# Kernel tuning notes

Measured on AMD Instinct MI355X. Metric: run time of the kernel, lower is better.

Reference implementation:

```python
import jax, jax.numpy as jnp
import numpy as np

STEP_NUM = 2
SAMPLE_NUM = 10
SAMPLE_SCOPE = 128
NODE_NUM = 232965
INPUT_DIM = 602
HIDDEN_DIM = 256
OUTPUT_DIM = 41
BATCH = 256


def _forward(ids, feature, edge, weight, sample_W, sample_W2, sample_a, W1, W2):
    # a: softmax over the 3 mixing coefficients (matches softmax_a(sample_a) then mm)
    a = jax.nn.softmax(sample_a, axis=0)[:, 0]  # [3]
    key = jax.random.key(42)
    adj_list = [None] * STEP_NUM
    in_nodes = ids
    for i in range(STEP_NUM):
        layer = STEP_NUM - 1 - i
        nbr = edge[in_nodes]              # [n, S] candidate neighbor ids
        src_f = feature[in_nodes]         # [n, F]
        tgt_f = feature[nbr]              # [n, S, F]
        # GAT-style bilinear attention scores (two heads) + structural weight
        s1 = src_f @ sample_W             # [n, H]
        s2 = src_f @ sample_W2            # [n, H]
        t1 = jnp.einsum('nsf,fh->nsh', tgt_f, sample_W)   # [n, S, H]
        t2 = jnp.einsum('nsf,fh->nsh', tgt_f, sample_W2)  # [n, S, H]
        att1 = jnp.einsum('nh,nsh->ns', s1, t1)
        att2 = jnp.einsum('nh,nsh->ns', s2, t2)
        att3 = weight[in_nodes]           # [n, S]
        att = jax.nn.relu(a[0] * att1 + a[1] * att2 + a[2] * att3) + 1e-9
        # Categorical sampling of SAMPLE_NUM neighbors per node
        key, sk = jax.random.split(key)
        cols = jax.random.categorical(sk, jnp.log(att), shape=(SAMPLE_NUM, in_nodes.shape[0])).T  # [n, K]
        # sub-graph adjacency: row-normalized sampled weights (block-sparse structure)
        w = jnp.take_along_axis(weight[in_nodes], cols, axis=1)  # [n, K]
        adj_list[layer] = w / (w.sum(axis=1, keepdims=True) + 1e-9)
        in_nodes = jnp.take_along_axis(nbr, cols, axis=1).reshape(-1)  # [n*K]
    X = feature[in_nodes]                 # start_feat: deepest frontier features
    Ws = [W1, W2]
    for layer in range(STEP_NUM):
        n = adj_list[layer].shape[0]
        # sparse adjacency matmul == per-row weighted sum over sampled neighbors
        X = jnp.einsum('nk,nkd->nd', adj_list[layer], X.reshape(n, SAMPLE_NUM, -1))
        X = X @ Ws[layer]
        if layer < STEP_NUM - 1:
            X = jax.nn.relu(X)  # dropout is identity in eval
    return X


def setup_inputs() -> dict:
    key = jax.random.key(0)
    ks = jax.random.split(key, 9)
    N1 = NODE_NUM + 1
    return {
        'ids': jax.random.randint(ks[0], (BATCH,), 0, NODE_NUM),
        'feature': jax.random.normal(ks[1], (N1, INPUT_DIM), dtype=jnp.float32),
        'edge': jax.random.randint(ks[2], (N1, SAMPLE_SCOPE), 0, NODE_NUM),
        'weight': jax.random.uniform(ks[3], (N1, SAMPLE_SCOPE), dtype=jnp.float32),
        'sample_W': jax.random.normal(ks[4], (INPUT_DIM, HIDDEN_DIM), dtype=jnp.float32) * 0.05,
        'sample_W2': jax.random.normal(ks[5], (INPUT_DIM, HIDDEN_DIM), dtype=jnp.float32) * 0.05,
        'sample_a': jax.random.normal(ks[6], (3, 1), dtype=jnp.float32),
        'W1': jax.random.normal(ks[7], (INPUT_DIM, HIDDEN_DIM), dtype=jnp.float32) * 0.05,
        'W2': jax.random.normal(ks[8], (HIDDEN_DIM, OUTPUT_DIM), dtype=jnp.float32) * 0.05,
    }


def reference(ids, feature, edge, weight, sample_W, sample_W2, sample_a, W1, W2):
    return _forward(ids, feature, edge, weight, sample_W, sample_W2, sample_a, W1, W2)
```

## Files before the change

### kernel.cpp

```cpp
#include <hip/hip_runtime.h>
#include <cstdint>
#include <cstddef>

#define JAX_PARTITIONABLE 1

#define S_SCOPE 128
#define K_SAMP  10
#define F_DIM   602
#define H_DIM   256
#define O_DIM   41
#define BATCH_N 256

__host__ __device__ __forceinline__ void tf2x32(uint32_t k0, uint32_t k1,
                                                uint32_t x0, uint32_t x1,
                                                uint32_t* o0, uint32_t* o1) {
  uint32_t ks2 = k0 ^ k1 ^ 0x1BD11BDAu;
  x0 += k0; x1 += k1;
#define TF_R(d) { x0 += x1; x1 = (x1 << (d)) | (x1 >> (32 - (d))); x1 ^= x0; }
#define TF_G0 TF_R(13) TF_R(15) TF_R(26) TF_R(6)
#define TF_G1 TF_R(17) TF_R(29) TF_R(16) TF_R(24)
  TF_G0; x0 += k1;  x1 += ks2 + 1u;
  TF_G1; x0 += ks2; x1 += k0  + 2u;
  TF_G0; x0 += k0;  x1 += k1  + 3u;
  TF_G1; x0 += k1;  x1 += ks2 + 4u;
  TF_G0; x0 += ks2; x1 += k0  + 5u;
#undef TF_R
#undef TF_G0
#undef TF_G1
  *o0 = x0; *o1 = x1;
}

__device__ __forceinline__ float jax_gumbel(uint32_t ka, uint32_t kb, uint32_t j, uint32_t M) {
  uint32_t r0, r1, bits;
#if JAX_PARTITIONABLE
  tf2x32(ka, kb, 0u, j, &r0, &r1);
  bits = r0 ^ r1;
#else
  uint32_t half = M >> 1;
  if (j < half) { tf2x32(ka, kb, j, j + half, &r0, &r1); bits = r0; }
  else          { tf2x32(ka, kb, j - half, j, &r0, &r1); bits = r1; }
#endif
  float f = __uint_as_float((bits >> 9) | 0x3f800000u) - 1.0f;
  if (f == 0.0f) f = 1.17549435e-38f;
  return -logf(-logf(f));
}

template<int R>
__global__ void __launch_bounds__(256) k_sg(const float* __restrict__ feature,
                                            const float* __restrict__ Wa,
                                            const float* __restrict__ Wb,
                                            const int* __restrict__ nodes,
                                            float* __restrict__ g1,
                                            float* __restrict__ g2) {
  __shared__ __align__(16) float fl[R][604];
  __shared__ __align__(16) float sl[R][H_DIM];
  const float* __restrict__ W = blockIdx.y ? Wb : Wa;
  float* __restrict__ g = blockIdx.y ? g2 : g1;
  const int r0 = blockIdx.x * R;
  const int tid = threadIdx.x;
  for (int r = 0; r < R; ++r) {
    const float* src = feature + (size_t)nodes[r0 + r] * F_DIM;
    for (int e = tid; e < 604; e += 256) fl[r][e] = (e < F_DIM) ? src[e] : 0.f;
  }
  __syncthreads();

  {
    const int h = tid;
    float a[R];
#pragma unroll
    for (int r = 0; r < R; ++r) a[r] = 0.f;
    for (int fc = 0; fc < 150; ++fc) {
      const int f = fc * 4;
      const float w0 = W[(size_t)(f + 0) * H_DIM + h];
      const float w1 = W[(size_t)(f + 1) * H_DIM + h];
      const float w2 = W[(size_t)(f + 2) * H_DIM + h];
      const float w3 = W[(size_t)(f + 3) * H_DIM + h];
#pragma unroll
      for (int r = 0; r < R; ++r) {
        const float4 v = *(const float4*)&fl[r][f];
        a[r] = fmaf(v.x, w0, a[r]); a[r] = fmaf(v.y, w1, a[r]);
        a[r] = fmaf(v.z, w2, a[r]); a[r] = fmaf(v.w, w3, a[r]);
      }
    }
    for (int f = 600; f < 602; ++f) {
      const float w = W[(size_t)f * H_DIM + h];
#pragma unroll
      for (int r = 0; r < R; ++r) a[r] = fmaf(fl[r][f], w, a[r]);
    }
#pragma unroll
    for (int r = 0; r < R; ++r) sl[r][h] = a[r];
  }
  __syncthreads();

  for (int j = 0; j < 3; ++j) {
    const int f = tid + j * 256;
    if (f < F_DIM) {
      const float4* wr = (const float4*)(W + (size_t)f * H_DIM);
      float b[R];
#pragma unroll
      for (int r = 0; r < R; ++r) b[r] = 0.f;
      for (int hq = 0; hq < H_DIM / 4; ++hq) {
        const float4 w = wr[hq];
#pragma unroll
        for (int r = 0; r < R; ++r) {
          const float4 v = *(const float4*)&sl[r][hq * 4];
          b[r] = fmaf(v.x, w.x, b[r]); b[r] = fmaf(v.y, w.y, b[r]);
          b[r] = fmaf(v.z, w.z, b[r]); b[r] = fmaf(v.w, w.w, b[r]);
        }
      }
#pragma unroll
      for (int r = 0; r < R; ++r)
        g[(size_t)(r0 + r) * F_DIM + f] = b[r];
    }
  }
}

template<int FUSE_Y, int BLK>
__global__ void __launch_bounds__(BLK) k_att(const float* __restrict__ feature,
                                             const int* __restrict__ edge,
                                             const float* __restrict__ weight,
                                             const float* __restrict__ g1,
                                             const float* __restrict__ g2,
                                             const int* __restrict__ nodes,
                                             int n,
                                             const float* __restrict__ sample_a,
                                             uint32_t ska, uint32_t skb,
                                             float* __restrict__ adj_or_y,
                                             int* __restrict__ out_nodes) {
  constexpr int NW = BLK / 64;
  __shared__ __align__(16) float g1l[602];
  __shared__ __align__(16) float g2l[602];
  __shared__ float logitl[S_SCOPE];
  __shared__ float wtl[S_SCOPE];
  __shared__ int nbrl[S_SCOPE];
  __shared__ int coll[K_SAMP];
  __shared__ float selw[K_SAMP];
  __shared__ int selr[K_SAMP];

  const int nIdx = blockIdx.x;
  const int tid = threadIdx.x;
  const int lane = tid & 63;
  const int wave = tid >> 6;
  const int node = nodes[nIdx];

  const float a0v = sample_a[0], a1v = sample_a[1], a2v = sample_a[2];
  const float mx = fmaxf(a0v, fmaxf(a1v, a2v));
  const float e0 = expf(a0v - mx), e1 = expf(a1v - mx), e2 = expf(a2v - mx);
  const float inv = 1.0f / (e0 + e1 + e2);
  const float aw0 = e0 * inv, aw1 = e1 * inv, aw2 = e2 * inv;

  for (int e = tid; e < F_DIM; e += BLK) {
    g1l[e] = g1[(size_t)nIdx * F_DIM + e];
    g2l[e] = g2[(size_t)nIdx * F_DIM + e];
  }
  __syncthreads();

  for (int t16 = 0; t16 < S_SCOPE / (2 * NW); ++t16) {
    const int sA = wave + t16 * (2 * NW);
    const int sB = sA + NW;
    const int nbrA = edge[(size_t)node * S_SCOPE + sA];
    const int nbrB = edge[(size_t)node * S_SCOPE + sB];
    const float wtA = weight[(size_t)node * S_SCOPE + sA];
    const float wtB = weight[(size_t)node * S_SCOPE + sB];
    const float2* frA = (const float2*)(feature + (size_t)nbrA * F_DIM);
    const float2* frB = (const float2*)(feature + (size_t)nbrB * F_DIM);
    float2 vA[5], vB[5], gav[5], gbv[5];
#pragma unroll
    for (int t = 0; t < 5; ++t) {
      const int p = lane + t * 64;
      if (p < F_DIM / 2) {
        vA[t] = frA[p]; vB[t] = frB[p];
        gav[t] = ((const float2*)g1l)[p];
        gbv[t] = ((const float2*)g2l)[p];
      } else {
        vA[t] = make_float2(0.f, 0.f); vB[t] = make_float2(0.f, 0.f);
        gav[t] = make_float2(0.f, 0.f); gbv[t] = make_float2(0.f, 0.f);
      }
    }
    float d1A = 0.f, d2A = 0.f, d1B = 0.f, d2B = 0.f;
#pragma unroll
    for (int t = 0; t < 5; ++t) {
      d1A = fmaf(vA[t].x, gav[t].x, fmaf(vA[t].y, gav[t].y, d1A));
      d2A = fmaf(vA[t].x, gbv[t].x, fmaf(vA[t].y, gbv[t].y, d2A));
      d1B = fmaf(vB[t].x, gav[t].x, fmaf(vB[t].y, gav[t].y, d1B));
      d2B = fmaf(vB[t].x, gbv[t].x, fmaf(vB[t].y, gbv[t].y, d2B));
    }
#pragma unroll
    for (int off = 32; off > 0; off >>= 1) {
      d1A += __shfl_xor(d1A, off); d2A += __shfl_xor(d2A, off);
      d1B += __shfl_xor(d1B, off); d2B += __shfl_xor(d2B, off);
    }
    if (lane == 0) {
      const float attA = fmaxf(aw0 * d1A + aw1 * d2A + aw2 * wtA, 0.0f) + 1e-9f;
      const float attB = fmaxf(aw0 * d1B + aw1 * d2B + aw2 * wtB, 0.0f) + 1e-9f;
      logitl[sA] = logf(attA); wtl[sA] = wtA; nbrl[sA] = nbrA;
      logitl[sB] = logf(attB); wtl[sB] = wtB; nbrl[sB] = nbrB;
    }
  }
  __syncthreads();

  const uint32_t M = (uint32_t)K_SAMP * (uint32_t)n * (uint32_t)S_SCOPE;
  for (int k = wave; k < K_SAMP; k += NW) {
    const uint32_t jbase = ((uint32_t)k * (uint32_t)n + (uint32_t)nIdx) * (uint32_t)S_SCOPE;
    float v0 = logitl[lane]      + jax_gumbel(ska, skb, jbase + (uint32_t)lane,        M);
    float v1 = logitl[lane + 64] + jax_gumbel(ska, skb, jbase + (uint32_t)(lane + 64), M);
    float best = v0; int bidx = lane;
    if (v1 > best) { best = v1; bidx = lane + 64; }
#pragma unroll
    for (int off = 1; off < 64; off <<= 1) {
      const float ov = __shfl_xor(best, off);
      const int oi = __shfl_xor(bidx, off);
      if (ov > best || (ov == best && oi < bidx)) { best = ov; bidx = oi; }
    }
    if (lane == 0) coll[k] = bidx;
  }
  __syncthreads();

  if constexpr (FUSE_Y) {
    if (tid == 0) {
      float w[K_SAMP]; float sum = 0.f;
#pragma unroll
      for (int k = 0; k < K_SAMP; ++k) { w[k] = wtl[coll[k]]; sum += w[k]; }
      const float den = sum + 1e-9f;
#pragma unroll
      for (int k = 0; k < K_SAMP; ++k) {
        selw[k] = w[k] / den;
        selr[k] = nbrl[coll[k]];
      }
    }
    __syncthreads();
    for (int e = tid; e < F_DIM; e += BLK) {
      float acc = 0.f;
#pragma unroll
      for (int k = 0; k < K_SAMP; ++k)
        acc = fmaf(selw[k], feature[(size_t)selr[k] * F_DIM + e], acc);
      adj_or_y[(size_t)nIdx * F_DIM + e] = acc;
    }
  } else {
    if (tid == 0) {
      float w[K_SAMP]; float sum = 0.f;
#pragma unroll
      for (int k = 0; k < K_SAMP; ++k) { w[k] = wtl[coll[k]]; sum += w[k]; }
      const float den = sum + 1e-9f;
#pragma unroll
      for (int k = 0; k < K_SAMP; ++k) {
        adj_or_y[(size_t)nIdx * K_SAMP + k] = w[k] / den;
        out_nodes[nIdx * K_SAMP + k] = nbrl[coll[k]];
      }
    }
  }
}

#define HROWS 4
__global__ void __launch_bounds__(256) k_h(const float* __restrict__ y,
                                           const float* __restrict__ W1,
                                           float* __restrict__ H) {
  __shared__ __align__(16) float yl[HROWS][604];
  const int r0 = blockIdx.x * HROWS;
  const int tid = threadIdx.x;
  for (int r = 0; r < HROWS; ++r)
    for (int e = tid; e < 604; e += 256)
      yl[r][e] = (e < F_DIM) ? y[(size_t)(r0 + r) * F_DIM + e] : 0.f;
  __syncthreads();
  const int h = tid;
  float acc[HROWS];
#pragma unroll
  for (int r = 0; r < HROWS; ++r) acc[r] = 0.f;
  for (int fc = 0; fc < 150; ++fc) {
    const int f = fc * 4;
    const float w0 = W1[(size_t)(f + 0) * H_DIM + h];
    const float w1 = W1[(size_t)(f + 1) * H_DIM + h];
    const float w2 = W1[(size_t)(f + 2) * H_DIM + h];
    const float w3 = W1[(size_t)(f + 3) * H_DIM + h];
#pragma unroll
    for (int r = 0; r < HROWS; ++r) {
      const float4 v = *(const float4*)&yl[r][f];
      acc[r] = fmaf(v.x, w0, acc[r]); acc[r] = fmaf(v.y, w1, acc[r]);
      acc[r] = fmaf(v.z, w2, acc[r]); acc[r] = fmaf(v.w, w3, acc[r]);
    }
  }
  for (int f = 600; f < 602; ++f) {
    const float w = W1[(size_t)f * H_DIM + h];
#pragma unroll
    for (int r = 0; r < HROWS; ++r) acc[r] = fmaf(yl[r][f], w, acc[r]);
  }
#pragma unroll
  for (int r = 0; r < HROWS; ++r)
    H[(size_t)(r0 + r) * H_DIM + h] = fmaxf(acc[r], 0.f);
}

__global__ void __launch_bounds__(256) k_final(const float* __restrict__ H,
                                               const float* __restrict__ adj1,
                                               const float* __restrict__ W2,
                                               float* __restrict__ out) {
  __shared__ float zl[H_DIM];
  const int nIdx = blockIdx.x;
  const int tid = threadIdx.x;
  float acc = 0.f;
#pragma unroll
  for (int k = 0; k < K_SAMP; ++k)
    acc = fmaf(adj1[(size_t)nIdx * K_SAMP + k],
               H[(size_t)(nIdx * K_SAMP + k) * H_DIM + tid], acc);
  zl[tid] = acc;
  __syncthreads();
  if (tid < O_DIM) {
    float o = 0.f;
    for (int hh = 0; hh < H_DIM; ++hh)
      o = fmaf(zl[hh], W2[(size_t)hh * O_DIM + tid], o);
    out[(size_t)nIdx * O_DIM + tid] = o;
  }
}

extern "C" void kernel_launch(void* const* d_in, const int* in_sizes, int n_in,
                              void* d_out, int out_size, void* d_ws, size_t ws_size,
                              hipStream_t stream) {
  (void)in_sizes; (void)n_in; (void)out_size; (void)ws_size;
  const int*   ids       = (const int*)d_in[0];
  const float* feature   = (const float*)d_in[1];
  const int*   edge      = (const int*)d_in[2];
  const float* weight    = (const float*)d_in[3];
  const float* sample_W  = (const float*)d_in[4];
  const float* sample_W2 = (const float*)d_in[5];
  const float* sample_a  = (const float*)d_in[6];
  const float* W1        = (const float*)d_in[7];
  const float* W2        = (const float*)d_in[8];
  float* out = (float*)d_out;

  const int N1 = BATCH_N;
  const int N2 = BATCH_N * K_SAMP;

  float* ws   = (float*)d_ws;
  float* g1   = ws;
  float* g2   = g1 + (size_t)N2 * F_DIM;
  float* yb   = g2 + (size_t)N2 * F_DIM;
  float* Hb   = yb + (size_t)N2 * F_DIM;
  float* adj1 = Hb + (size_t)N2 * H_DIM;
  int*   in1  = (int*)(adj1 + (size_t)N1 * K_SAMP);

  uint32_t k0 = 0u, k1 = 42u;
  uint32_t nk0, nk1, sk0a, sk0b, sk1a, sk1b;
#if JAX_PARTITIONABLE
  {
    tf2x32(k0, k1, 0u, 0u, &nk0, &nk1);
    tf2x32(k0, k1, 0u, 1u, &sk0a, &sk0b);
    tf2x32(nk0, nk1, 0u, 1u, &sk1a, &sk1b);
  }
#else
  {
    uint32_t a0, b0, a1, b1;
    tf2x32(k0, k1, 0u, 2u, &a0, &b0);
    tf2x32(k0, k1, 1u, 3u, &a1, &b1);
    nk0 = a0; nk1 = a1; sk0a = b0; sk0b = b1;
    tf2x32(nk0, nk1, 0u, 2u, &a0, &b0);
    tf2x32(nk0, nk1, 1u, 3u, &a1, &b1);
    sk1a = b0; sk1b = b1;
  }
#endif

  k_sg<2><<<dim3(N1 / 2, 2), 256, 0, stream>>>(feature, sample_W, sample_W2, ids, g1, g2);
  k_att<0, 1024><<<N1, 1024, 0, stream>>>(feature, edge, weight, g1, g2, ids, N1,
                                          sample_a, sk0a, sk0b, adj1, in1);
  k_sg<10><<<dim3(N2 / 10, 2), 256, 0, stream>>>(feature, sample_W, sample_W2, in1, g1, g2);
  k_att<1, 512><<<N2, 512, 0, stream>>>(feature, edge, weight, g1, g2, in1, N2,
                                        sample_a, sk1a, sk1b, yb, nullptr);
  k_h<<<N2 / HROWS, 256, 0, stream>>>(yb, W1, Hb);
  k_final<<<N1, 256, 0, stream>>>(Hb, adj1, W2, out);
}
```

Baseline: 369.9 us.

## Fuse layer-0 projection with attention, pipeline neighbor loads, fuse output kernels

Merges the first-hop sg projection into the first attention kernel, so each block computes its own g1/g2 vectors in shared memory. The attention core now preloads edge and weight rows once and double-buffers the neighbor feature rows, overlapping the next row's load with the current dot product. It also fuses the hidden projection, ReLU, weighted aggregation and output matmul into one kernel, removing the H buffer round trip. The cost is redundant W reads per block in the fused layer-0 kernel and the 1024-thread layer-0 launch being cut to 512 threads.

```diff
diff --git a/kernel.cpp b/kernel.cpp
--- a/kernel.cpp
+++ b/kernel.cpp
@@ -45,6 +45,224 @@
   return -logf(-logf(f));
 }
 
+__device__ __forceinline__ void cand_load(const float* __restrict__ feature,
+                                          int nbr, int lane, float2* buf) {
+  const float2* fr = (const float2*)(feature + (size_t)nbr * F_DIM);
+#pragma unroll
+  for (int t = 0; t < 5; ++t) {
+    const int p = lane + t * 64;
+    buf[t] = (p < F_DIM / 2) ? fr[p] : make_float2(0.f, 0.f);
+  }
+}
+
+__device__ __forceinline__ void cand_dot(const float2* buf,
+                                         const float* g1l, const float* g2l,
+                                         int lane, float& d1, float& d2) {
+  d1 = 0.f; d2 = 0.f;
+#pragma unroll
+  for (int t = 0; t < 5; ++t) {
+    const int p = lane + t * 64;
+    float2 ga, gb;
+    if (p < F_DIM / 2) {
+      ga = ((const float2*)g1l)[p];
+      gb = ((const float2*)g2l)[p];
+    } else {
+      ga = make_float2(0.f, 0.f);
+      gb = make_float2(0.f, 0.f);
+    }
+    d1 = fmaf(buf[t].x, ga.x, fmaf(buf[t].y, ga.y, d1));
+    d2 = fmaf(buf[t].x, gb.x, fmaf(buf[t].y, gb.y, d2));
+  }
+}
+
+__device__ __forceinline__ void red2(float& d1, float& d2) {
+#pragma unroll
+  for (int off = 32; off > 0; off >>= 1) {
+    d1 += __shfl_xor(d1, off);
+    d2 += __shfl_xor(d2, off);
+  }
+}
+
+template<int FUSE_Y>
+__device__ __forceinline__ void att_core(const float* __restrict__ feature,
+                                         const float* g1l, const float* g2l,
+                                         float* logitl, float* wtl, int* nbrl,
+                                         int* coll, float* selw, int* selr,
+                                         int nIdx, int n,
+                                         float aw0, float aw1, float aw2,
+                                         uint32_t ska, uint32_t skb,
+                                         float* __restrict__ adj_or_y,
+                                         int* __restrict__ out_nodes) {
+  constexpr int BLK = 512;
+  constexpr int NW = BLK / 64;
+  constexpr int NIT = S_SCOPE / NW;
+  const int tid = threadIdx.x;
+  const int lane = tid & 63;
+  const int wave = tid >> 6;
+
+  float2 bufA[5], bufB[5];
+  cand_load(feature, nbrl[wave], lane, bufA);
+  for (int it = 0; it < NIT; it += 2) {
+    const int sA = wave + it * NW;
+    const int sB = sA + NW;
+    cand_load(feature, nbrl[sB], lane, bufB);
+    {
+      float d1, d2;
+      cand_dot(bufA, g1l, g2l, lane, d1, d2);
+      red2(d1, d2);
+      if (lane == 0) {
+        const float att = fmaxf(aw0 * d1 + aw1 * d2 + aw2 * wtl[sA], 0.0f) + 1e-9f;
+        logitl[sA] = logf(att);
+      }
+    }
+    if (it + 2 < NIT) cand_load(feature, nbrl[sB + NW], lane, bufA);
+    {
+      float d1, d2;
+      cand_dot(bufB, g1l, g2l, lane, d1, d2);
+      red2(d1, d2);
+      if (lane == 0) {
+        const float att = fmaxf(aw0 * d1 + aw1 * d2 + aw2 * wtl[sB], 0.0f) + 1e-9f;
+        logitl[sB] = logf(att);
+      }
+    }
+  }
+  __syncthreads();
+
+  const uint32_t M = (uint32_t)K_SAMP * (uint32_t)n * (uint32_t)S_SCOPE;
+  for (int k = wave; k < K_SAMP; k += NW) {
+    const uint32_t jbase = ((uint32_t)k * (uint32_t)n + (uint32_t)nIdx) * (uint32_t)S_SCOPE;
+    float v0 = logitl[lane]      + jax_gumbel(ska, skb, jbase + (uint32_t)lane,        M);
+    float v1 = logitl[lane + 64] + jax_gumbel(ska, skb, jbase + (uint32_t)(lane + 64), M);
+    float best = v0; int bidx = lane;
+    if (v1 > best) { best = v1; bidx = lane + 64; }
+#pragma unroll
+    for (int off = 1; off < 64; off <<= 1) {
+      const float ov = __shfl_xor(best, off);
+      const int oi = __shfl_xor(bidx, off);
+      if (ov > best || (ov == best && oi < bidx)) { best = ov; bidx = oi; }
+    }
+    if (lane == 0) coll[k] = bidx;
+  }
+  __syncthreads();
+
+  if constexpr (FUSE_Y) {
+    if (tid == 0) {
+      float w[K_SAMP]; float sum = 0.f;
+#pragma unroll
+      for (int k = 0; k < K_SAMP; ++k) { w[k] = wtl[coll[k]]; sum += w[k]; }
+      const float den = sum + 1e-9f;
+#pragma unroll
+      for (int k = 0; k < K_SAMP; ++k) {
+        selw[k] = w[k] / den;
+        selr[k] = nbrl[coll[k]];
+      }
+    }
+    __syncthreads();
+    for (int e = tid; e < F_DIM; e += BLK) {
+      float acc = 0.f;
+#pragma unroll
+      for (int k = 0; k < K_SAMP; ++k)
+        acc = fmaf(selw[k], feature[(size_t)selr[k] * F_DIM + e], acc);
+      adj_or_y[(size_t)nIdx * F_DIM + e] = acc;
+    }
+  } else {
+    if (tid == 0) {
+      float w[K_SAMP]; float sum = 0.f;
+#pragma unroll
+      for (int k = 0; k < K_SAMP; ++k) { w[k] = wtl[coll[k]]; sum += w[k]; }
+      const float den = sum + 1e-9f;
+#pragma unroll
+      for (int k = 0; k < K_SAMP; ++k) {
+        adj_or_y[(size_t)nIdx * K_SAMP + k] = w[k] / den;
+        out_nodes[nIdx * K_SAMP + k] = nbrl[coll[k]];
+      }
+    }
+  }
+}
+
+__global__ void __launch_bounds__(512) k_sgatt0(const float* __restrict__ feature,
+                                                const int* __restrict__ edge,
+                                                const float* __restrict__ weight,
+                                                const float* __restrict__ Wa,
+                                                const float* __restrict__ Wb,
+                                                const int* __restrict__ nodes,
+                                                int n,
+                                                const float* __restrict__ sample_a,
+                                                uint32_t ska, uint32_t skb,
+                                                float* __restrict__ adj,
+                                                int* __restrict__ out_nodes) {
+  __shared__ __align__(16) float fl[604];
+  __shared__ __align__(16) float sl[2][H_DIM];
+  __shared__ __align__(16) float g1l[604];
+  __shared__ __align__(16) float g2l[604];
+  __shared__ float logitl[S_SCOPE];
+  __shared__ float wtl[S_SCOPE];
+  __shared__ int nbrl[S_SCOPE];
+  __shared__ int coll[K_SAMP];
+
+  const int nIdx = blockIdx.x;
+  const int tid = threadIdx.x;
+  const int node = nodes[nIdx];
+
+  const float a0v = sample_a[0], a1v = sample_a[1], a2v = sample_a[2];
+  const float mx = fmaxf(a0v, fmaxf(a1v, a2v));
+  const float e0 = expf(a0v - mx), e1 = expf(a1v - mx), e2 = expf(a2v - mx);
+  const float inv = 1.0f / (e0 + e1 + e2);
+  const float aw0 = e0 * inv, aw1 = e1 * inv, aw2 = e2 * inv;
+
+  {
+    const float* src = feature + (size_t)node * F_DIM;
+    for (int e = tid; e < 604; e += 512) fl[e] = (e < F_DIM) ? src[e] : 0.f;
+    if (tid < S_SCOPE) {
+      nbrl[tid] = edge[(size_t)node * S_SCOPE + tid];
+      wtl[tid] = weight[(size_t)node * S_SCOPE + tid];
+    }
+  }
+  __syncthreads();
+
+  {
+    const int head = tid >> 8;
+    const int h = tid & 255;
+    const float* __restrict__ W = head ? Wb : Wa;
+    float a = 0.f;
+    for (int fc = 0; fc < 150; ++fc) {
+      const int f = fc * 4;
+      const float w0 = W[(size_t)(f + 0) * H_DIM + h];
+      const float w1 = W[(size_t)(f + 1) * H_DIM + h];
+      const float w2 = W[(size_t)(f + 2) * H_DIM + h];
+      const float w3 = W[(size_t)(f + 3) * H_DIM + h];
+      const float4 v = *(const float4*)&fl[f];
+      a = fmaf(v.x, w0, a); a = fmaf(v.y, w1, a);
+      a = fmaf(v.z, w2, a); a = fmaf(v.w, w3, a);
+    }
+    for (int f = 600; f < 602; ++f) a = fmaf(fl[f], W[(size_t)f * H_DIM + h], a);
+    sl[head][h] = a;
+  }
+  __syncthreads();
+
+  for (int j = 0; j < 3; ++j) {
+    const int idx = tid + j * 512;
+    if (idx < 2 * F_DIM) {
+      const int head = idx >= F_DIM;
+      const int f = head ? idx - F_DIM : idx;
+      const float* __restrict__ W = head ? Wb : Wa;
+      const float4* wr = (const float4*)(W + (size_t)f * H_DIM);
+      float b = 0.f;
+      for (int hq = 0; hq < H_DIM / 4; ++hq) {
+        const float4 w = wr[hq];
+        const float4 v = *(const float4*)&sl[head][hq * 4];
+        b = fmaf(v.x, w.x, b); b = fmaf(v.y, w.y, b);
+        b = fmaf(v.z, w.z, b); b = fmaf(v.w, w.w, b);
+      }
+      (head ? g2l : g1l)[f] = b;
+    }
+  }
+  __syncthreads();
+
+  att_core<0>(feature, g1l, g2l, logitl, wtl, nbrl, coll, nullptr, nullptr,
+              nIdx, n, aw0, aw1, aw2, ska, skb, adj, out_nodes);
+}
+
 template<int R>
 __global__ void __launch_bounds__(256) k_sg(const float* __restrict__ feature,
                                             const float* __restrict__ Wa,
@@ -115,21 +333,18 @@
   }
 }
 
-template<int FUSE_Y, int BLK>
-__global__ void __launch_bounds__(BLK) k_att(const float* __restrict__ feature,
-                                             const int* __restrict__ edge,
-                                             const float* __restrict__ weight,
-                                             const float* __restrict__ g1,
-                                             const float* __restrict__ g2,
-                                             const int* __restrict__ nodes,
-                                             int n,
-                                             const float* __restrict__ sample_a,
-                                             uint32_t ska, uint32_t skb,
-                                             float* __restrict__ adj_or_y,
-                                             int* __restrict__ out_nodes) {
-  constexpr int NW = BLK / 64;
-  __shared__ __align__(16) float g1l[602];
-  __shared__ __align__(16) float g2l[602];
+__global__ void __launch_bounds__(512) k_att1(const float* __restrict__ feature,
+                                              const int* __restrict__ edge,
+                                              const float* __restrict__ weight,
+                                              const float* __restrict__ g1,
+                                              const float* __restrict__ g2,
+                                              const int* __restrict__ nodes,
+                                              int n,
+                                              const float* __restrict__ sample_a,
+                                              uint32_t ska, uint32_t skb,
+                                              float* __restrict__ y) {
+  __shared__ __align__(16) float g1l[604];
+  __shared__ __align__(16) float g2l[604];
   __shared__ float logitl[S_SCOPE];
   __shared__ float wtl[S_SCOPE];
   __shared__ int nbrl[S_SCOPE];
@@ -139,8 +354,6 @@
 
   const int nIdx = blockIdx.x;
   const int tid = threadIdx.x;
-  const int lane = tid & 63;
-  const int wave = tid >> 6;
   const int node = nodes[nIdx];
 
   const float a0v = sample_a[0], a1v = sample_a[1], a2v = sample_a[2];
@@ -149,123 +362,39 @@
   const float inv = 1.0f / (e0 + e1 + e2);
   const float aw0 = e0 * inv, aw1 = e1 * inv, aw2 = e2 * inv;
 
-  for (int e = tid; e < F_DIM; e += BLK) {
+  for (int e = tid; e < F_DIM; e += 512) {
     g1l[e] = g1[(size_t)nIdx * F_DIM + e];
     g2l[e] = g2[(size_t)nIdx * F_DIM + e];
   }
-  __syncthreads();
-
-  for (int t16 = 0; t16 < S_SCOPE / (2 * NW); ++t16) {
-    const int sA = wave + t16 * (2 * NW);
-    const int sB = sA + NW;
-    const int nbrA = edge[(size_t)node * S_SCOPE + sA];
-    const int nbrB = edge[(size_t)node * S_SCOPE + sB];
-    const float wtA = weight[(size_t)node * S_SCOPE + sA];
-    const float wtB = weight[(size_t)node * S_SCOPE + sB];
-    const float2* frA = (const float2*)(feature + (size_t)nbrA * F_DIM);
-    const float2* frB = (const float2*)(feature + (size_t)nbrB * F_DIM);
-    float2 vA[5], vB[5], gav[5], gbv[5];
-#pragma unroll
-    for (int t = 0; t < 5; ++t) {
-      const int p = lane + t * 64;
-      if (p < F_DIM / 2) {
-        vA[t] = frA[p]; vB[t] = frB[p];
-        gav[t] = ((const float2*)g1l)[p];
-        gbv[t] = ((const float2*)g2l)[p];
-      } else {
-        vA[t] = make_float2(0.f, 0.f); vB[t] = make_float2(0.f, 0.f);
-        gav[t] = make_float2(0.f, 0.f); gbv[t] = make_float2(0.f, 0.f);
-      }
-    }
-    float d1A = 0.f, d2A = 0.f, d1B = 0.f, d2B = 0.f;
-#pragma unroll
-    for (int t = 0; t < 5; ++t) {
-      d1A = fmaf(vA[t].x, gav[t].x, fmaf(vA[t].y, gav[t].y, d1A));
-      d2A = fmaf(vA[t].x, gbv[t].x, fmaf(vA[t].y, gbv[t].y, d2A));
-      d1B = fmaf(vB[t].x, gav[t].x, fmaf(vB[t].y, gav[t].y, d1B));
-      d2B = fmaf(vB[t].x, gbv[t].x, fmaf(vB[t].y, gbv[t].y, d2B));
-    }
-#pragma unroll
-    for (int off = 32; off > 0; off >>= 1) {
-      d1A += __shfl_xor(d1A, off); d2A += __shfl_xor(d2A, off);
-      d1B += __shfl_xor(d1B, off); d2B += __shfl_xor(d2B, off);
-    }
-    if (lane == 0) {
-      const float attA = fmaxf(aw0 * d1A + aw1 * d2A + aw2 * wtA, 0.0f) + 1e-9f;
-      const float attB = fmaxf(aw0 * d1B + aw1 * d2B + aw2 * wtB, 0.0f) + 1e-9f;
-      logitl[sA] = logf(attA); wtl[sA] = wtA; nbrl[sA] = nbrA;
-      logitl[sB] = logf(attB); wtl[sB] = wtB; nbrl[sB] = nbrB;
-    }
-  }
-  __syncthreads();
-
-  const uint32_t M = (uint32_t)K_SAMP * (uint32_t)n * (uint32_t)S_SCOPE;
-  for (int k = wave; k < K_SAMP; k += NW) {
-    const uint32_t jbase = ((uint32_t)k * (uint32_t)n + (uint32_t)nIdx) * (uint32_t)S_SCOPE;
-    float v0 = logitl[lane]      + jax_gumbel(ska, skb, jbase + (uint32_t)lane,        M);
-    float v1 = logitl[lane + 64] + jax_gumbel(ska, skb, jbase + (uint32_t)(lane + 64), M);
-    float best = v0; int bidx = lane;
-    if (v1 > best) { best = v1; bidx = lane + 64; }
-#pragma unroll
-    for (int off = 1; off < 64; off <<= 1) {
-      const float ov = __shfl_xor(best, off);
-      const int oi = __shfl_xor(bidx, off);
-      if (ov > best || (ov == best && oi < bidx)) { best = ov; bidx = oi; }
-    }
-    if (lane == 0) coll[k] = bidx;
-  }
-  __syncthreads();
-
-  if constexpr (FUSE_Y) {
-    if (tid == 0) {
-      float w[K_SAMP]; float sum = 0.f;
-#pragma unroll
-      for (int k = 0; k < K_SAMP; ++k) { w[k] = wtl[coll[k]]; sum += w[k]; }
-      const float den = sum + 1e-9f;
-#pragma unroll
-      for (int k = 0; k < K_SAMP; ++k) {
-        selw[k] = w[k] / den;
-        selr[k] = nbrl[coll[k]];
-      }
-    }
-    __syncthreads();
-    for (int e = tid; e < F_DIM; e += BLK) {
-      float acc = 0.f;
-#pragma unroll
-      for (int k = 0; k < K_SAMP; ++k)
-        acc = fmaf(selw[k], feature[(size_t)selr[k] * F_DIM + e], acc);
-      adj_or_y[(size_t)nIdx * F_DIM + e] = acc;
-    }
-  } else {
-    if (tid == 0) {
-      float w[K_SAMP]; float sum = 0.f;
-#pragma unroll
-      for (int k = 0; k < K_SAMP; ++k) { w[k] = wtl[coll[k]]; sum += w[k]; }
-      const float den = sum + 1e-9f;
-#pragma unroll
-      for (int k = 0; k < K_SAMP; ++k) {
-        adj_or_y[(size_t)nIdx * K_SAMP + k] = w[k] / den;
-        out_nodes[nIdx * K_SAMP + k] = nbrl[coll[k]];
-      }
-    }
-  }
-}
-
-#define HROWS 4
-__global__ void __launch_bounds__(256) k_h(const float* __restrict__ y,
-                                           const float* __restrict__ W1,
-                                           float* __restrict__ H) {
-  __shared__ __align__(16) float yl[HROWS][604];
-  const int r0 = blockIdx.x * HROWS;
+  if (tid < S_SCOPE) {
+    nbrl[tid] = edge[(size_t)node * S_SCOPE + tid];
+    wtl[tid] = weight[(size_t)node * S_SCOPE + tid];
+  }
+  __syncthreads();
+
+  att_core<1>(feature, g1l, g2l, logitl, wtl, nbrl, coll, selw, selr,
+              nIdx, n, aw0, aw1, aw2, ska, skb, y, nullptr);
+}
+
+__global__ void __launch_bounds__(256) k_out(const float* __restrict__ y,
+                                             const float* __restrict__ W1,
+                                             const float* __restrict__ adj1,
+                                             const float* __restrict__ W2,
+                                             float* __restrict__ out) {
+  __shared__ __align__(16) float yl[K_SAMP][604];
+  __shared__ float zl[H_DIM];
+  const int nIdx = blockIdx.x;
+  const int r0 = nIdx * K_SAMP;
   const int tid = threadIdx.x;
-  for (int r = 0; r < HROWS; ++r)
+  for (int r = 0; r < K_SAMP; ++r)
     for (int e = tid; e < 604; e += 256)
       yl[r][e] = (e < F_DIM) ? y[(size_t)(r0 + r) * F_DIM + e] : 0.f;
   __syncthreads();
+
   const int h = tid;
-  float acc[HROWS];
-#pragma unroll
-  for (int r = 0; r < HROWS; ++r) acc[r] = 0.f;
+  float acc[K_SAMP];
+#pragma unroll
+  for (int r = 0; r < K_SAMP; ++r) acc[r] = 0.f;
   for (int fc = 0; fc < 150; ++fc) {
     const int f = fc * 4;
     const float w0 = W1[(size_t)(f + 0) * H_DIM + h];
@@ -273,7 +402,7 @@
     const float w2 = W1[(size_t)(f + 2) * H_DIM + h];
     const float w3 = W1[(size_t)(f + 3) * H_DIM + h];
 #pragma unroll
-    for (int r = 0; r < HROWS; ++r) {
+    for (int r = 0; r < K_SAMP; ++r) {
       const float4 v = *(const float4*)&yl[r][f];
       acc[r] = fmaf(v.x, w0, acc[r]); acc[r] = fmaf(v.y, w1, acc[r]);
       acc[r] = fmaf(v.z, w2, acc[r]); acc[r] = fmaf(v.w, w3, acc[r]);
@@ -282,27 +411,16 @@
   for (int f = 600; f < 602; ++f) {
     const float w = W1[(size_t)f * H_DIM + h];
 #pragma unroll
-    for (int r = 0; r < HROWS; ++r) acc[r] = fmaf(yl[r][f], w, acc[r]);
-  }
-#pragma unroll
-  for (int r = 0; r < HROWS; ++r)
-    H[(size_t)(r0 + r) * H_DIM + h] = fmaxf(acc[r], 0.f);
-}
-
-__global__ void __launch_bounds__(256) k_final(const float* __restrict__ H,
-                                               const float* __restrict__ adj1,
-                                               const float* __restrict__ W2,
-                                               float* __restrict__ out) {
-  __shared__ float zl[H_DIM];
-  const int nIdx = blockIdx.x;
-  const int tid = threadIdx.x;
-  float acc = 0.f;
+    for (int r = 0; r < K_SAMP; ++r) acc[r] = fmaf(yl[r][f], w, acc[r]);
+  }
+
+  float z = 0.f;
 #pragma unroll
   for (int k = 0; k < K_SAMP; ++k)
-    acc = fmaf(adj1[(size_t)nIdx * K_SAMP + k],
-               H[(size_t)(nIdx * K_SAMP + k) * H_DIM + tid], acc);
-  zl[tid] = acc;
-  __syncthreads();
+    z = fmaf(adj1[(size_t)nIdx * K_SAMP + k], fmaxf(acc[k], 0.f), z);
+  zl[h] = z;
+  __syncthreads();
+
   if (tid < O_DIM) {
     float o = 0.f;
     for (int hh = 0; hh < H_DIM; ++hh)
@@ -333,8 +451,7 @@
   float* g1   = ws;
   float* g2   = g1 + (size_t)N2 * F_DIM;
   float* yb   = g2 + (size_t)N2 * F_DIM;
-  float* Hb   = yb + (size_t)N2 * F_DIM;
-  float* adj1 = Hb + (size_t)N2 * H_DIM;
+  float* adj1 = yb + (size_t)N2 * F_DIM;
   int*   in1  = (int*)(adj1 + (size_t)N1 * K_SAMP);
 
   uint32_t k0 = 0u, k1 = 42u;
@@ -357,12 +474,10 @@
   }
 #endif
 
-  k_sg<2><<<dim3(N1 / 2, 2), 256, 0, stream>>>(feature, sample_W, sample_W2, ids, g1, g2);
-  k_att<0, 1024><<<N1, 1024, 0, stream>>>(feature, edge, weight, g1, g2, ids, N1,
-                                          sample_a, sk0a, sk0b, adj1, in1);
+  k_sgatt0<<<N1, 512, 0, stream>>>(feature, edge, weight, sample_W, sample_W2,
+                                   ids, N1, sample_a, sk0a, sk0b, adj1, in1);
   k_sg<10><<<dim3(N2 / 10, 2), 256, 0, stream>>>(feature, sample_W, sample_W2, in1, g1, g2);
-  k_att<1, 512><<<N2, 512, 0, stream>>>(feature, edge, weight, g1, g2, in1, N2,
-                                        sample_a, sk1a, sk1b, yb, nullptr);
-  k_h<<<N2 / HROWS, 256, 0, stream>>>(yb, W1, Hb);
-  k_final<<<N1, 256, 0, stream>>>(Hb, adj1, W2, out);
-}
+  k_att1<<<N2, 512, 0, stream>>>(feature, edge, weight, g1, g2, in1, N2,
+                                 sample_a, sk1a, sk1b, yb);
+  k_out<<<N1, 256, 0, stream>>>(yb, W1, adj1, W2, out);
+}
```

New measurement: 397.5 us. 1.07x slower.
